# Kernel optimization log

Hardware: AMD Instinct MI355X
Metric: run time of the kernel (lower is better)

The kernel has to match this reference:

```python
import jax, jax.numpy as jnp
import numpy as np

B, OPI, RPI = 8, 64, 1024        # images, objects/image, rels/image
N, R = B * OPI, B * RPI           # 512 objects, 8192 relations
OBJ_DIM, H, T = 4096, 512, 3
NOC, NRC = 151, 51
IOU_THR = 0.3


def setup_inputs() -> dict:
    key = jax.random.key(0)
    ks = jax.random.split(key, 30)
    im_inds = jnp.repeat(jnp.arange(B, dtype=jnp.int64), OPI)
    rel_im = jnp.repeat(jnp.arange(B, dtype=jnp.int64), RPI)
    sub = rel_im * OPI + jax.random.randint(ks[0], (R,), 0, OPI)
    obj = rel_im * OPI + jax.random.randint(ks[1], (R,), 0, OPI)
    rel_inds = jnp.stack([rel_im, sub, obj], axis=1)
    obj_fmaps = jax.random.normal(ks[2], (N, OBJ_DIM), jnp.float32)
    obj_logits = jax.random.normal(ks[3], (N, NOC), jnp.float32)
    vr = jax.random.normal(ks[4], (R, OBJ_DIM), jnp.float32)
    xy = jax.random.uniform(ks[5], (N, NOC, 2), jnp.float32) * 500.0
    wh = jax.random.uniform(ks[6], (N, NOC, 2), jnp.float32) * 100.0 + 1.0
    boxes_per_cls = jnp.concatenate([xy, xy + wh], axis=-1)  # valid x1y1x2y2

    def lin(k, i, o):
        return jax.random.normal(k, (i, o), jnp.float32) / np.sqrt(i).astype(np.float32)

    params = dict(
        W_obj_proj=lin(ks[7], OBJ_DIM, H), b_obj_proj=jnp.zeros((H,), jnp.float32),
        W_rel_proj=lin(ks[8], OBJ_DIM, H), b_rel_proj=jnp.zeros((H,), jnp.float32),
        W_emb=lin(ks[9], NOC, H),
        W_msg_rel=lin(ks[10], H, H), W_msg_obj=lin(ks[11], H, H),
        W_gru_obj=lin(ks[12], H, 3 * H), U_gru_obj=lin(ks[13], H, 3 * H), b_gru_obj=jnp.zeros((3 * H,), jnp.float32),
        W_gru_rel=lin(ks[14], H, 3 * H), U_gru_rel=lin(ks[15], H, 3 * H), b_gru_rel=jnp.zeros((3 * H,), jnp.float32),
        W_cls_rel=lin(ks[16], H, NRC), b_cls_rel=jnp.zeros((NRC,), jnp.float32),
        W_cls_obj=lin(ks[17], H, NOC), b_cls_obj=jnp.zeros((NOC,), jnp.float32),
    )
    return dict(im_inds=im_inds, obj_fmaps=obj_fmaps, obj_logits=obj_logits,
                rel_inds=rel_inds, vr=vr, boxes_per_cls=boxes_per_cls, **params)


def _gru(h, x, W, U, b):
    g = jax.nn.sigmoid(x @ W[:, :2 * H] + h @ U[:, :2 * H] + b[:2 * H])
    z, r = jnp.split(g, 2, axis=-1)
    n = jnp.tanh(x @ W[:, 2 * H:] + (r * h) @ U[:, 2 * H:] + b[2 * H:])
    return (1.0 - z) * h + z * n


def _ggnn_image(rel_pair, obj_probs, obj_f, vr_im, W_emb, W_msg_rel, W_msg_obj,
                W_gru_obj, U_gru_obj, b_gru_obj, W_gru_rel, U_gru_rel, b_gru_rel,
                W_cls_rel, b_cls_rel, W_cls_obj, b_cls_obj):
    # object node init: projected features + class-prob embedding; rel nodes from vr
    h_obj = obj_f + obj_probs @ W_emb           # [OPI, H]
    h_rel = vr_im                                # [RPI, H]
    s, o = rel_pair[:, 0], rel_pair[:, 1]
    for _ in range(T):
        m_rel = (h_obj[s] + h_obj[o]) @ W_msg_rel
        hm = h_rel @ W_msg_obj
        m_obj = jnp.zeros_like(h_obj).at[s].add(hm).at[o].add(hm)
        h_rel = _gru(h_rel, m_rel, W_gru_rel, U_gru_rel, b_gru_rel)
        h_obj = _gru(h_obj, m_obj, W_gru_obj, U_gru_obj, b_gru_obj)
    return h_rel @ W_cls_rel + b_cls_rel, h_obj @ W_cls_obj + b_cls_obj


def _nms_keep(boxes, scores):
    # greedy NMS, iou_threshold=0.3; returns bool keep mask [N]
    order = jnp.argsort(-scores)
    b = boxes[order]
    area = (b[:, 2] - b[:, 0]) * (b[:, 3] - b[:, 1])
    lt = jnp.maximum(b[:, None, :2], b[None, :, :2])
    rb = jnp.minimum(b[:, None, 2:], b[None, :, 2:])
    wh = jnp.clip(rb - lt, 0.0)
    inter = wh[..., 0] * wh[..., 1]
    iou = inter / (area[:, None] + area[None, :] - inter + 1e-9)
    idx = jnp.arange(N)

    def body(i, keep):
        sup = keep[i] & (iou[i] > IOU_THR) & (idx > i)
        return keep & ~sup

    keep_sorted = jax.lax.fori_loop(0, N, body, jnp.ones((N,), bool))
    return jnp.zeros((N,), bool).at[order].set(keep_sorted)


def reference(im_inds, obj_fmaps, obj_logits, rel_inds, vr, boxes_per_cls,
              W_obj_proj, b_obj_proj, W_rel_proj, b_rel_proj, W_emb,
              W_msg_rel, W_msg_obj, W_gru_obj, U_gru_obj, b_gru_obj,
              W_gru_rel, U_gru_rel, b_gru_rel, W_cls_rel, b_cls_rel,
              W_cls_obj, b_cls_obj):
    obj_probs = jax.nn.softmax(obj_logits, axis=-1)
    fo = obj_fmaps @ W_obj_proj + b_obj_proj      # [N, H]
    vrp = vr @ W_rel_proj + b_rel_proj            # [R, H]
    # local object indices per image (rel_inds[:,1:] - obj_s), ragged -> uniform reshape
    rel_local = (rel_inds[:, 1:] - rel_inds[:, 0:1] * OPI).reshape(B, RPI, 2)
    ggnn = jax.vmap(_ggnn_image, in_axes=(0, 0, 0, 0) + (None,) * 13)
    rel_logits, obj_ref = ggnn(rel_local, obj_probs.reshape(B, OPI, NOC),
                               fo.reshape(B, OPI, H), vrp.reshape(B, RPI, H),
                               W_emb, W_msg_rel, W_msg_obj,
                               W_gru_obj, U_gru_obj, b_gru_obj,
                               W_gru_rel, U_gru_rel, b_gru_rel,
                               W_cls_rel, b_cls_rel, W_cls_obj, b_cls_obj)
    rel_logits = rel_logits.reshape(R, NRC)
    obj_logits_out = obj_ref.reshape(N, NOC)      # refine_obj_cls=True path
    obj_probs2 = jax.nn.softmax(obj_logits_out, axis=-1)
    # sgdet eval: per-class NMS (classes 1..NOC-1), vectorized over classes
    sp = jax.lax.stop_gradient(obj_probs2)        # .data in torch
    keep = jax.vmap(_nms_keep, in_axes=(1, 1))(boxes_per_cls[:, 1:], sp[:, 1:])  # [NOC-1, N]
    nms_mask = jnp.zeros((N, NOC), jnp.float32).at[:, 1:].set(keep.T.astype(jnp.float32))
    obj_preds = jnp.argmax((nms_mask * sp)[:, 1:], axis=1) + 1
    return obj_logits_out, obj_preds, rel_logits
```

## Files before the change

### kernel.cpp

```cpp
#include <hip/hip_runtime.h>
#include <math.h>

#define OPI 64
#define RPI 1024
#define N_OBJ 512
#define R_REL 8192
#define OBJ_DIM 4096
#define H 512
#define NOC 151
#define NRC 51
#define T_ITERS 3
#define IOU_THRESH 0.3f

typedef unsigned short u16;
typedef unsigned int u32;
typedef __attribute__((ext_vector_type(4))) float f32x4;
typedef __attribute__((ext_vector_type(8))) short bf16x8;
typedef __attribute__((ext_vector_type(2))) unsigned int u32x2;
typedef __attribute__((ext_vector_type(8))) short s16x8;

enum { EPI_STORE = 0, EPI_BIAS = 1, EPI_GATE = 3, EPI_NEWH = 4 };

__device__ inline u16 f2bf(float x) {
  u32 u = __float_as_uint(x);
  u32 r = (u + 0x7fffu + ((u >> 16) & 1u)) >> 16;
  return (u16)r;
}
__device__ inline float bf2f(u16 h) { return __uint_as_float(((u32)h) << 16); }
__device__ inline u32 cvtpk(float a, float b) {
  u32 r;
  asm("v_cvt_pk_bf16_f32 %0, %1, %2" : "=v"(r) : "v"(a), "v"(b));
  return r;
}

__global__ __launch_bounds__(256) void prep_bt(
    const float* __restrict__ W1, int ld1, int K1,
    const float* __restrict__ W2, int ld2, int K2,
    int coloff, int ncols, int N, int Kpad,
    u16* __restrict__ outh, u16* __restrict__ outl)
{
  __shared__ float tile[64][65];
  const int k0 = blockIdx.x * 64;
  const int n0 = blockIdx.y * 64;
  const int t = threadIdx.x;
  const int lane = t & 63;
  const int w = t >> 6;
#pragma unroll
  for (int p = 0; p < 16; ++p) {
    int kl = w * 16 + p;
    int k = k0 + kl;
    int n = n0 + lane;
    float v = 0.f;
    if (n < ncols) {
      if (k < K1) v = W1[(size_t)k * ld1 + coloff + n];
      else if (k - K1 < K2) v = W2[(size_t)(k - K1) * ld2 + coloff + n];
    }
    tile[kl][lane] = v;
  }
  __syncthreads();
#pragma unroll
  for (int p = 0; p < 16; ++p) {
    int nl = w * 16 + p;
    int n = n0 + nl;
    int k = k0 + lane;
    if (n < N && k < Kpad) {
      float v = tile[lane][nl];
      u16 h = f2bf(v);
      outh[(size_t)n * Kpad + k] = h;
      outl[(size_t)n * Kpad + k] = f2bf(v - bf2f(h));
    }
  }
}

template<int EPI, bool DUAL, bool GATHER, bool PAIR, bool SPLIT>
__global__ __launch_bounds__(256, 2) void mgemm_k(
    int M, int N, int K1, int K2, int nkt,
    const float* __restrict__ A1, int lda1,
    const float* __restrict__ A2, int lda2,
    const u16* __restrict__ Bth, const u16* __restrict__ Btl,
    const u16* __restrict__ Bth2, const u16* __restrict__ Btl2,
    const float* __restrict__ bias,
    float* __restrict__ C, int ldc, float* __restrict__ C2,
    const int* __restrict__ ridx,
    const float* __restrict__ Hb, int ldh,
    const float* __restrict__ Zin,
    float* __restrict__ Zout, float* __restrict__ RHout,
    float* __restrict__ part, int ktchunk)
{
  __shared__ u16 lAh[2][128 * 32];
  __shared__ u16 lAl[2][128 * 32];
  __shared__ u16 lBh[2][128 * 32];
  __shared__ u16 lBl[2][128 * 32];
  const int t = threadIdx.x;
  const int lane = t & 63;
  const int wid = t >> 6;
  const int wm = wid >> 1;
  const int wn = wid & 1;

  const int nbx = gridDim.x, nby = gridDim.y;
  const int nwg = nbx * nby;
  int orig = blockIdx.y * nbx + blockIdx.x;
  int lid = (orig & 7) * (nwg >> 3) + (orig >> 3);
  const int bx = lid % nbx;
  const int by = lid / nbx;

  const int m0 = by * 128;
  const int n0 = bx * 128;
  const int Kpad = nkt * 32;

  const float* A1p = A1; int ldap = lda1;
  const u16* Bhp = Bth; const u16* Blp = Btl;
  float* Cp = C;
  bool gath = GATHER;
  if (PAIR && blockIdx.z == 1) {
    A1p = A2; ldap = lda2; Bhp = Bth2; Blp = Btl2; Cp = C2; gath = false;
  }

  f32x4 acc[4][4];
#pragma unroll
  for (int m = 0; m < 4; ++m)
#pragma unroll
    for (int n = 0; n < 4; ++n) acc[m][n] = f32x4{0.f, 0.f, 0.f, 0.f};

  const int a_row = t >> 3;
  const int a_kq  = t & 7;
  int g_si[4], g_oi[4];
  if (gath) {
#pragma unroll
    for (int i = 0; i < 4; ++i) {
      int gm = m0 + a_row + i * 32;
      g_si[i] = ridx[gm * 3 + 1];
      g_oi[i] = ridx[gm * 3 + 2];
    }
  }
  const int b_row  = t >> 2;
  const int b_slot = t & 3;

  int ktb = 0, kte = nkt;
  if (SPLIT) {
    ktb = blockIdx.z * ktchunk;
    kte = min(nkt, ktb + ktchunk);
  }

  float4 rA[4];
  s16x8 rBh[2], rBl[2];

  auto loadA = [&](int kt) {
    const int gk = kt * 32 + a_kq * 4;
#pragma unroll
    for (int i = 0; i < 4; ++i) {
      const int gm = m0 + a_row + i * 32;
      if (gath) {
        float4 va = *(const float4*)&A1p[(size_t)g_si[i] * ldap + gk];
        float4 vb = *(const float4*)&A1p[(size_t)g_oi[i] * ldap + gk];
        rA[i] = make_float4(va.x + vb.x, va.y + vb.y, va.z + vb.z, va.w + vb.w);
      } else if (!DUAL) {
        rA[i] = *(const float4*)&A1p[(size_t)gm * ldap + gk];
      } else {
        if (gk + 3 < K1) {
          rA[i] = *(const float4*)&A1p[(size_t)gm * lda1 + gk];
        } else if (gk >= K1 && gk + 3 < K1 + K2 && (lda2 & 3) == 0) {
          rA[i] = *(const float4*)&A2[(size_t)gm * lda2 + (gk - K1)];
        } else {
          float xs[4];
#pragma unroll
          for (int e = 0; e < 4; ++e) {
            int gke = gk + e;
            float xv = 0.f;
            if (gke < K1) xv = A1p[(size_t)gm * lda1 + gke];
            else if (gke < K1 + K2) xv = A2[(size_t)gm * lda2 + (gke - K1)];
            xs[e] = xv;
          }
          rA[i] = make_float4(xs[0], xs[1], xs[2], xs[3]);
        }
      }
    }
  };
  auto loadB = [&](int kt) {
#pragma unroll
    for (int i = 0; i < 2; ++i) {
      const size_t goff = (size_t)(n0 + b_row + i * 64) * Kpad + kt * 32 + b_slot * 8;
      rBh[i] = *(const s16x8*)&Bhp[goff];
      rBl[i] = *(const s16x8*)&Blp[goff];
    }
  };
  auto stage = [&](int buf) {
#pragma unroll
    for (int i = 0; i < 4; ++i) {
      const int row = a_row + i * 32;
      float x0 = rA[i].x, x1 = rA[i].y, x2 = rA[i].z, x3 = rA[i].w;
      u32 h01 = cvtpk(x0, x1);
      u32 h23 = cvtpk(x2, x3);
      float r0 = __uint_as_float(h01 << 16);
      float r1 = __uint_as_float(h01 & 0xffff0000u);
      float r2 = __uint_as_float(h23 << 16);
      float r3 = __uint_as_float(h23 & 0xffff0000u);
      u32 l01 = cvtpk(x0 - r0, x1 - r1);
      u32 l23 = cvtpk(x2 - r2, x3 - r3);
      const int base = row * 32 + (((a_kq >> 1) ^ ((row >> 1) & 3)) << 3) + (a_kq & 1) * 4;
      *reinterpret_cast<u32x2*>(&lAh[buf][base]) = u32x2{h01, h23};
      *reinterpret_cast<u32x2*>(&lAl[buf][base]) = u32x2{l01, l23};
    }
#pragma unroll
    for (int i = 0; i < 2; ++i) {
      const int row = b_row + i * 64;
      const int base = row * 32 + ((b_slot ^ ((row >> 1) & 3)) << 3);
      *reinterpret_cast<s16x8*>(&lBh[buf][base]) = rBh[i];
      *reinterpret_cast<s16x8*>(&lBl[buf][base]) = rBl[i];
    }
  };

  const int fr = lane & 15;
  const int kg = lane >> 4;

  if (ktb < kte) {
    loadA(ktb);
    loadB(ktb);
    stage(0);
    __syncthreads();
    const int nk = kte - ktb;
    for (int kk = 0; kk < nk; ++kk) {
      const int cur = kk & 1;
      const bool more = (kk + 1 < nk);
      if (more) { loadA(ktb + kk + 1); loadB(ktb + kk + 1); }
      bf16x8 ah[4], al[4], bh[4], bl[4];
#pragma unroll
      for (int m = 0; m < 4; ++m) {
        const int r = wm * 64 + m * 16 + fr;
        const int addr = r * 32 + ((kg ^ ((r >> 1) & 3)) << 3);
        ah[m] = *reinterpret_cast<const bf16x8*>(&lAh[cur][addr]);
        al[m] = *reinterpret_cast<const bf16x8*>(&lAl[cur][addr]);
      }
#pragma unroll
      for (int n = 0; n < 4; ++n) {
        const int r = wn * 64 + n * 16 + fr;
        const int addr = r * 32 + ((kg ^ ((r >> 1) & 3)) << 3);
        bh[n] = *reinterpret_cast<const bf16x8*>(&lBh[cur][addr]);
        bl[n] = *reinterpret_cast<const bf16x8*>(&lBl[cur][addr]);
      }
      __builtin_amdgcn_s_setprio(1);
#pragma unroll
      for (int m = 0; m < 4; ++m)
#pragma unroll
        for (int n = 0; n < 4; ++n) {
          acc[m][n] = __builtin_amdgcn_mfma_f32_16x16x32_bf16(ah[m], bh[n], acc[m][n], 0, 0, 0);
          acc[m][n] = __builtin_amdgcn_mfma_f32_16x16x32_bf16(ah[m], bl[n], acc[m][n], 0, 0, 0);
          acc[m][n] = __builtin_amdgcn_mfma_f32_16x16x32_bf16(al[m], bh[n], acc[m][n], 0, 0, 0);
        }
      __builtin_amdgcn_s_setprio(0);
      if (more) stage(cur ^ 1);
      __syncthreads();
    }
  }

  const int col = lane & 15;
  const int rb = (lane >> 4) * 4;
  if (SPLIT) {
    const int Npad = gridDim.x * 128;
    float* pp = part + (size_t)blockIdx.z * M * Npad;
#pragma unroll
    for (int m = 0; m < 4; ++m)
#pragma unroll
      for (int n = 0; n < 4; ++n) {
        const int gn = n0 + wn * 64 + n * 16 + col;
#pragma unroll
        for (int j = 0; j < 4; ++j) {
          const int gm = m0 + wm * 64 + m * 16 + rb + j;
          pp[(size_t)gm * Npad + gn] = acc[m][n][j];
        }
      }
    return;
  }
#pragma unroll
  for (int m = 0; m < 4; ++m) {
#pragma unroll
    for (int n = 0; n < 4; ++n) {
      const int gn = n0 + wn * 64 + n * 16 + col;
      if (gn >= N) continue;
#pragma unroll
      for (int j = 0; j < 4; ++j) {
        const int gm = m0 + wm * 64 + m * 16 + rb + j;
        float v = acc[m][n][j];
        if (EPI == EPI_STORE) {
          Cp[(size_t)gm * ldc + gn] = v;
        } else if (EPI == EPI_BIAS) {
          Cp[(size_t)gm * ldc + gn] = v + bias[gn];
        } else if (EPI == EPI_GATE) {
          float g = 1.f / (1.f + expf(-(v + bias[gn])));
          int half = N >> 1;
          if (gn < half) Zout[(size_t)gm * half + gn] = g;
          else RHout[(size_t)gm * half + (gn - half)] = g * Hb[(size_t)gm * ldh + (gn - half)];
        } else if (EPI == EPI_NEWH) {
          float nv = tanhf(v + bias[gn]);
          float z = Zin[(size_t)gm * N + gn];
          float h = Hb[(size_t)gm * ldh + gn];
          Cp[(size_t)gm * ldc + gn] = (1.f - z) * h + z * nv;
        }
      }
    }
  }
}

template<int EPI>
__global__ __launch_bounds__(256) void epi_reduce(
    int S, int M, int N, int Npad,
    const float* __restrict__ part, const float* __restrict__ bias,
    float* __restrict__ C, int ldc,
    const float* __restrict__ Hb, int ldh,
    const float* __restrict__ Zin,
    float* __restrict__ Zout, float* __restrict__ RHout)
{
  int idx = blockIdx.x * 256 + threadIdx.x;
  if (idx >= M * Npad) return;
  int m = idx / Npad;
  int n = idx - m * Npad;
  if (n >= N) return;
  size_t stride = (size_t)M * Npad;
  float v = 0.f;
  for (int s = 0; s < S; ++s) v += part[s * stride + idx];
  if (EPI == EPI_BIAS) {
    C[(size_t)m * ldc + n] = v + bias[n];
  } else if (EPI == EPI_GATE) {
    float g = 1.f / (1.f + expf(-(v + bias[n])));
    int half = N >> 1;
    if (n < half) Zout[(size_t)m * half + n] = g;
    else RHout[(size_t)m * half + (n - half)] = g * Hb[(size_t)m * ldh + (n - half)];
  } else if (EPI == EPI_NEWH) {
    float nv = tanhf(v + bias[n]);
    float z = Zin[(size_t)m * N + n];
    float h = Hb[(size_t)m * ldh + n];
    C[(size_t)m * ldc + n] = (1.f - z) * h + z * nv;
  }
}

__global__ __launch_bounds__(256) void softmax_k(const float* __restrict__ X,
                                                 float* __restrict__ P)
{
  int row = blockIdx.x;
  int t = threadIdx.x;
  __shared__ float red[4];
  float x = (t < NOC) ? X[row * NOC + t] : -3.4e38f;
  float m = x;
#pragma unroll
  for (int o = 32; o > 0; o >>= 1) m = fmaxf(m, __shfl_xor(m, o, 64));
  if ((t & 63) == 0) red[t >> 6] = m;
  __syncthreads();
  float mm = fmaxf(fmaxf(red[0], red[1]), fmaxf(red[2], red[3]));
  float e = (t < NOC) ? expf(x - mm) : 0.f;
  float s = e;
#pragma unroll
  for (int o = 32; o > 0; o >>= 1) s += __shfl_xor(s, o, 64);
  __syncthreads();
  if ((t & 63) == 0) red[t >> 6] = s;
  __syncthreads();
  float ss = red[0] + red[1] + red[2] + red[3];
  if (t < NOC) P[row * NOC + t] = e / ss;
}

__global__ __launch_bounds__(256) void m_obj_gather_k(const float* __restrict__ hm,
                                                      const int* __restrict__ ridx,
                                                      float* __restrict__ m_obj)
{
  int n = blockIdx.x;
  int im = n >> 6;
  int col = threadIdx.x;
  float acc0 = 0.f, acc1 = 0.f;
  int r0 = im * RPI, r1 = r0 + RPI;
  for (int r = r0; r < r1; ++r) {
    int s = ridx[r * 3 + 1];
    int o = ridx[r * 3 + 2];
    int cnt = (s == n) + (o == n);
    if (cnt) {
      float f = (float)cnt;
      acc0 = fmaf(f, hm[r * H + col], acc0);
      acc1 = fmaf(f, hm[r * H + col + 256], acc1);
    }
  }
  m_obj[n * H + col] = acc0;
  m_obj[n * H + col + 256] = acc1;
}

__global__ __launch_bounds__(512) void nms_k(const float* __restrict__ probs2,
                                             const float* __restrict__ boxes,
                                             float* __restrict__ keepmask)
{
  int c = blockIdx.x + 1;
  int t = threadIdx.x;
  __shared__ float sc[512];
  __shared__ int   si[512];
  __shared__ float bx0[512], by0[512], bx1[512], by1[512], sar[512];
  __shared__ int   skeep[512];

  sc[t] = probs2[t * NOC + c];
  si[t] = t;
  __syncthreads();

  for (int k = 2; k <= 512; k <<= 1) {
    for (int j = k >> 1; j > 0; j >>= 1) {
      int p = t ^ j;
      if (p > t) {
        float s1 = sc[t], s2 = sc[p];
        int   i1 = si[t], i2 = si[p];
        bool tBefore = (s1 > s2) || (s1 == s2 && i1 < i2);
        bool up = ((t & k) == 0);
        if (up != tBefore) { sc[t] = s2; sc[p] = s1; si[t] = i2; si[p] = i1; }
      }
      __syncthreads();
    }
  }

  {
    const float* b = &boxes[(si[t] * NOC + c) * 4];
    float x0 = b[0], y0 = b[1], x1 = b[2], y1 = b[3];
    bx0[t] = x0; by0[t] = y0; bx1[t] = x1; by1[t] = y1;
    sar[t] = (x1 - x0) * (y1 - y0);
    skeep[t] = 1;
  }
  __syncthreads();

  for (int i = 0; i < 511; ++i) {
    if (skeep[i] && t > i && skeep[t]) {
      float lx = fmaxf(bx0[i], bx0[t]);
      float ly = fmaxf(by0[i], by0[t]);
      float rx = fminf(bx1[i], bx1[t]);
      float ry = fminf(by1[i], by1[t]);
      float w = fmaxf(rx - lx, 0.f);
      float h = fmaxf(ry - ly, 0.f);
      float inter = w * h;
      float iou = inter / (sar[i] + sar[t] - inter + 1e-9f);
      if (iou > IOU_THRESH) skeep[t] = 0;
    }
    __syncthreads();
  }

  keepmask[(c - 1) * N_OBJ + si[t]] = skeep[t] ? 1.f : 0.f;
}

__global__ void pred_k(const float* __restrict__ probs2,
                       const float* __restrict__ keepmask,
                       float* __restrict__ out)
{
  int i = threadIdx.x + blockIdx.x * 256;
  if (i >= N_OBJ) return;
  float best = -1.f;
  int bc = 0;
  for (int c = 0; c < NOC - 1; ++c) {
    float v = keepmask[c * N_OBJ + i] * probs2[i * NOC + c + 1];
    if (v > best) { best = v; bc = c; }
  }
  out[i] = (float)(bc + 1);
}

extern "C" void kernel_launch(void* const* d_in, const int* in_sizes, int n_in,
                              void* d_out, int out_size, void* d_ws, size_t ws_size,
                              hipStream_t stream) {
  const float* obj_fmaps  = (const float*)d_in[1];
  const float* obj_logits = (const float*)d_in[2];
  const int*   rel_inds   = (const int*)d_in[3];
  const float* vr         = (const float*)d_in[4];
  const float* boxes      = (const float*)d_in[5];
  const float* W_obj_proj = (const float*)d_in[6];
  const float* b_obj_proj = (const float*)d_in[7];
  const float* W_rel_proj = (const float*)d_in[8];
  const float* b_rel_proj = (const float*)d_in[9];
  const float* W_emb      = (const float*)d_in[10];
  const float* W_msg_rel  = (const float*)d_in[11];
  const float* W_msg_obj  = (const float*)d_in[12];
  const float* W_gru_obj  = (const float*)d_in[13];
  const float* U_gru_obj  = (const float*)d_in[14];
  const float* b_gru_obj  = (const float*)d_in[15];
  const float* W_gru_rel  = (const float*)d_in[16];
  const float* U_gru_rel  = (const float*)d_in[17];
  const float* b_gru_rel  = (const float*)d_in[18];
  const float* W_cls_rel  = (const float*)d_in[19];
  const float* b_cls_rel  = (const float*)d_in[20];
  const float* W_cls_obj  = (const float*)d_in[21];
  const float* b_cls_obj  = (const float*)d_in[22];

  float* ws = (float*)d_ws;
  const size_t RH = (size_t)R_REL * H;
  const size_t NH = (size_t)N_OBJ * H;
  float* h_rel  = ws;
  float* m_rel  = h_rel  + RH;
  float* z_rel  = m_rel  + RH;
  float* rh_rel = z_rel  + RH;
  float* h_obj  = rh_rel + RH;
  float* m_obj  = h_obj  + NH;
  float* z_obj  = m_obj  + NH;
  float* rh_obj = z_obj  + NH;
  float* obj_probs  = rh_obj + NH;
  float* obj_probs2 = obj_probs  + (size_t)N_OBJ * NOC;
  float* keepmask   = obj_probs2 + (size_t)N_OBJ * NOC;
  float* hm   = z_rel;
  float* part = m_rel;
  float* fend = keepmask + (size_t)(NOC - 1) * N_OBJ;

  u16* bt = (u16*)fend;
  const int KP_HOBJ = 4256;
  const int KP_HREL = 4096;
  const int KP_MSG  = 512;
  const int KP_GRU  = 1024;
  const int KP_CLS  = 512;
  u16* p = bt;
  u16* bt_hobj_h = p; p += (size_t)H * KP_HOBJ;      u16* bt_hobj_l = p; p += (size_t)H * KP_HOBJ;
  u16* bt_hrel_h = p; p += (size_t)H * KP_HREL;      u16* bt_hrel_l = p; p += (size_t)H * KP_HREL;
  u16* bt_mrel_h = p; p += (size_t)H * KP_MSG;       u16* bt_mrel_l = p; p += (size_t)H * KP_MSG;
  u16* bt_hm_h   = p; p += (size_t)H * KP_MSG;       u16* bt_hm_l   = p; p += (size_t)H * KP_MSG;
  u16* bt_gr_h   = p; p += (size_t)2 * H * KP_GRU;   u16* bt_gr_l   = p; p += (size_t)2 * H * KP_GRU;
  u16* bt_nr_h   = p; p += (size_t)H * KP_GRU;       u16* bt_nr_l   = p; p += (size_t)H * KP_GRU;
  u16* bt_go_h   = p; p += (size_t)2 * H * KP_GRU;   u16* bt_go_l   = p; p += (size_t)2 * H * KP_GRU;
  u16* bt_no_h   = p; p += (size_t)H * KP_GRU;       u16* bt_no_l   = p; p += (size_t)H * KP_GRU;
  u16* bt_cr_h   = p; p += (size_t)128 * KP_CLS;     u16* bt_cr_l   = p; p += (size_t)128 * KP_CLS;
  u16* bt_co_h   = p; p += (size_t)256 * KP_CLS;     u16* bt_co_l   = p; p += (size_t)256 * KP_CLS;

  size_t used_b = (size_t)((char*)p - (char*)d_ws);
  used_b = (used_b + 15) & ~(size_t)15;
  float* part2 = (float*)((char*)d_ws + used_b);
  bool have2 = (used_b + 2 * RH * sizeof(float)) <= ws_size;

  float* out_logits = (float*)d_out;
  float* out_preds  = out_logits + (size_t)N_OBJ * NOC;
  float* out_rel    = out_preds + N_OBJ;

  dim3 blk(256);
#define PREP(W1, ld1, K1, W2, ld2, K2, coff, NC, NN, KP, oh, ol) \
  prep_bt<<<dim3(((KP) + 63) / 64, ((NN) + 63) / 64), 256, 0, stream>>>( \
      W1, ld1, K1, W2, ld2, K2, coff, NC, NN, KP, oh, ol)

  PREP(W_obj_proj, H, OBJ_DIM, W_emb, H, NOC, 0, H, H, KP_HOBJ, bt_hobj_h, bt_hobj_l);
  PREP(W_rel_proj, H, OBJ_DIM, (const float*)nullptr, 0, 0, 0, H, H, KP_HREL, bt_hrel_h, bt_hrel_l);
  PREP(W_msg_rel, H, H, (const float*)nullptr, 0, 0, 0, H, H, KP_MSG, bt_mrel_h, bt_mrel_l);
  PREP(W_msg_obj, H, H, (const float*)nullptr, 0, 0, 0, H, H, KP_MSG, bt_hm_h, bt_hm_l);
  PREP(W_gru_rel, 3 * H, H, U_gru_rel, 3 * H, H, 0, 2 * H, 2 * H, KP_GRU, bt_gr_h, bt_gr_l);
  PREP(W_gru_rel, 3 * H, H, U_gru_rel, 3 * H, H, 2 * H, H, H, KP_GRU, bt_nr_h, bt_nr_l);
  PREP(W_gru_obj, 3 * H, H, U_gru_obj, 3 * H, H, 0, 2 * H, 2 * H, KP_GRU, bt_go_h, bt_go_l);
  PREP(W_gru_obj, 3 * H, H, U_gru_obj, 3 * H, H, 2 * H, H, H, KP_GRU, bt_no_h, bt_no_l);
  PREP(W_cls_rel, NRC, H, (const float*)nullptr, 0, 0, 0, NRC, 128, KP_CLS, bt_cr_h, bt_cr_l);
  PREP(W_cls_obj, NOC, H, (const float*)nullptr, 0, 0, 0, NOC, 256, KP_CLS, bt_co_h, bt_co_l);

  softmax_k<<<N_OBJ, 256, 0, stream>>>(obj_logits, obj_probs);

#define MG(EPI, DUAL, GATH, PAIR, SPLIT, grid, M, N, K1, K2, nkt, A1, lda1, A2, lda2, \
           Bh, Bl, Bh2, Bl2, bias, C, ldc, C2, ridx, Hb, ldh, Zin, Zo, RHo, part, ktc) \
  mgemm_k<EPI, DUAL, GATH, PAIR, SPLIT><<<grid, blk, 0, stream>>>( \
      M, N, K1, K2, nkt, A1, lda1, A2, lda2, Bh, Bl, Bh2, Bl2, bias, C, ldc, C2, \
      ridx, Hb, ldh, Zin, Zo, RHo, part, ktc)

  MG(EPI_STORE, true, false, false, true, dim3(4, 4, 8), N_OBJ, H, OBJ_DIM, NOC, KP_HOBJ / 32,
     obj_fmaps, OBJ_DIM, obj_probs, NOC, bt_hobj_h, bt_hobj_l, nullptr, nullptr,
     nullptr, nullptr, 0, nullptr, nullptr, nullptr, 0, nullptr, nullptr, nullptr, part, 17);
  epi_reduce<EPI_BIAS><<<(N_OBJ * H + 255) / 256, blk, 0, stream>>>(
      8, N_OBJ, H, H, part, b_obj_proj, h_obj, H, nullptr, 0, nullptr, nullptr, nullptr);

  MG(EPI_STORE, false, false, false, true, dim3(4, 64, 2), R_REL, H, OBJ_DIM, 0, KP_HREL / 32,
     vr, OBJ_DIM, nullptr, 0, bt_hrel_h, bt_hrel_l, nullptr, nullptr,
     nullptr, nullptr, 0, nullptr, nullptr, nullptr, 0, nullptr, nullptr, nullptr, part, 64);
  epi_reduce<EPI_BIAS><<<((int)(RH) + 255) / 256, blk, 0, stream>>>(
      2, R_REL, H, H, part, b_rel_proj, h_rel, H, nullptr, 0, nullptr, nullptr, nullptr);

  for (int it = 0; it < T_ITERS; ++it) {
    MG(EPI_STORE, false, true, true, false, dim3(4, 64, 2), R_REL, H, H, 0, KP_MSG / 32,
       h_obj, H, h_rel, H, bt_mrel_h, bt_mrel_l, bt_hm_h, bt_hm_l,
       nullptr, m_rel, H, hm, rel_inds, nullptr, 0, nullptr, nullptr, nullptr, nullptr, 0);
    m_obj_gather_k<<<N_OBJ, 256, 0, stream>>>(hm, rel_inds, m_obj);

    MG(EPI_GATE, true, false, false, false, dim3(8, 64), R_REL, 2 * H, H, H, KP_GRU / 32,
       m_rel, H, h_rel, H, bt_gr_h, bt_gr_l, nullptr, nullptr,
       b_gru_rel, nullptr, 0, nullptr, nullptr, h_rel, H, nullptr, z_rel, rh_rel, nullptr, 0);
    if (have2) {
      MG(EPI_STORE, true, false, false, true, dim3(4, 64, 2), R_REL, H, H, H, KP_GRU / 32,
         m_rel, H, rh_rel, H, bt_nr_h, bt_nr_l, nullptr, nullptr,
         nullptr, nullptr, 0, nullptr, nullptr, nullptr, 0, nullptr, nullptr, nullptr, part2, 16);
      epi_reduce<EPI_NEWH><<<((int)(RH) + 255) / 256, blk, 0, stream>>>(
          2, R_REL, H, H, part2, b_gru_rel + 2 * H, h_rel, H, h_rel, H, z_rel, nullptr, nullptr);
    } else {
      MG(EPI_NEWH, true, false, false, false, dim3(4, 64), R_REL, H, H, H, KP_GRU / 32,
         m_rel, H, rh_rel, H, bt_nr_h, bt_nr_l, nullptr, nullptr,
         b_gru_rel + 2 * H, h_rel, H, nullptr, nullptr, h_rel, H, z_rel, nullptr, nullptr, nullptr, 0);
    }

    MG(EPI_STORE, true, false, false, true, dim3(8, 4, 8), N_OBJ, 2 * H, H, H, KP_GRU / 32,
       m_obj, H, h_obj, H, bt_go_h, bt_go_l, nullptr, nullptr,
       nullptr, nullptr, 0, nullptr, nullptr, nullptr, 0, nullptr, nullptr, nullptr, part, 4);
    epi_reduce<EPI_GATE><<<(N_OBJ * 2 * H + 255) / 256, blk, 0, stream>>>(
        8, N_OBJ, 2 * H, 2 * H, part, b_gru_obj, nullptr, 0, h_obj, H, nullptr, z_obj, rh_obj);
    MG(EPI_STORE, true, false, false, true, dim3(4, 4, 8), N_OBJ, H, H, H, KP_GRU / 32,
       m_obj, H, rh_obj, H, bt_no_h, bt_no_l, nullptr, nullptr,
       nullptr, nullptr, 0, nullptr, nullptr, nullptr, 0, nullptr, nullptr, nullptr, part, 4);
    epi_reduce<EPI_NEWH><<<(N_OBJ * H + 255) / 256, blk, 0, stream>>>(
        8, N_OBJ, H, H, part, b_gru_obj + 2 * H, h_obj, H, h_obj, H, z_obj, nullptr, nullptr);
  }

  MG(EPI_STORE, false, false, false, true, dim3(1, 64, 4), R_REL, NRC, H, 0, KP_CLS / 32,
     h_rel, H, nullptr, 0, bt_cr_h, bt_cr_l, nullptr, nullptr,
     nullptr, nullptr, 0, nullptr, nullptr, nullptr, 0, nullptr, nullptr, nullptr, part, 4);
  epi_reduce<EPI_BIAS><<<(R_REL * 128 + 255) / 256, blk, 0, stream>>>(
      4, R_REL, NRC, 128, part, b_cls_rel, out_rel, NRC, nullptr, 0, nullptr, nullptr, nullptr);
  MG(EPI_STORE, false, false, false, true, dim3(2, 4, 8), N_OBJ, NOC, H, 0, KP_CLS / 32,
     h_obj, H, nullptr, 0, bt_co_h, bt_co_l, nullptr, nullptr,
     nullptr, nullptr, 0, nullptr, nullptr, nullptr, 0, nullptr, nullptr, nullptr, part, 2);
  epi_reduce<EPI_BIAS><<<(N_OBJ * 256 + 255) / 256, blk, 0, stream>>>(
      8, N_OBJ, NOC, 256, part, b_cls_obj, out_logits, NOC, nullptr, 0, nullptr, nullptr, nullptr);

  softmax_k<<<N_OBJ, 256, 0, stream>>>(out_logits, obj_probs2);
  nms_k<<<NOC - 1, 512, 0, stream>>>(obj_probs2, boxes, keepmask);
  pred_k<<<2, 256, 0, stream>>>(obj_probs2, keepmask, out_preds);
}
```

Before: 1.522 ms.

## Replace barrier-per-box NMS loop with bitmask IoU matrix and single-wave resolve

The old NMS ran 511 serial steps, each ending in a block-wide barrier. Now every thread first computes its row of the pairwise IoU matrix against all other boxes and packs the suppression results into 64-bit words in shared memory. A single wavefront then resolves the keep bits by walking the boxes in order, using lane shuffles and no block barriers. This removes most of the synchronisation, but it computes the full 512x512 IoU matrix (more divides) and uses more shared memory, and the resolve step is still a 512-step serial chain.

```diff
diff --git a/kernel.cpp b/kernel.cpp
--- a/kernel.cpp
+++ b/kernel.cpp
@@ -14,6 +14,7 @@
 
 typedef unsigned short u16;
 typedef unsigned int u32;
+typedef unsigned long long u64;
 typedef __attribute__((ext_vector_type(4))) float f32x4;
 typedef __attribute__((ext_vector_type(8))) short bf16x8;
 typedef __attribute__((ext_vector_type(2))) unsigned int u32x2;
@@ -389,7 +390,8 @@
   __shared__ float sc[512];
   __shared__ int   si[512];
   __shared__ float bx0[512], by0[512], bx1[512], by1[512], sar[512];
-  __shared__ int   skeep[512];
+  __shared__ u64   msk[512][8];
+  __shared__ u64   keepw_s[8];
 
   sc[t] = probs2[t * NOC + c];
   si[t] = t;
@@ -414,26 +416,48 @@
     float x0 = b[0], y0 = b[1], x1 = b[2], y1 = b[3];
     bx0[t] = x0; by0[t] = y0; bx1[t] = x1; by1[t] = y1;
     sar[t] = (x1 - x0) * (y1 - y0);
-    skeep[t] = 1;
-  }
-  __syncthreads();
-
-  for (int i = 0; i < 511; ++i) {
-    if (skeep[i] && t > i && skeep[t]) {
-      float lx = fmaxf(bx0[i], bx0[t]);
-      float ly = fmaxf(by0[i], by0[t]);
-      float rx = fminf(bx1[i], bx1[t]);
-      float ry = fminf(by1[i], by1[t]);
-      float w = fmaxf(rx - lx, 0.f);
-      float h = fmaxf(ry - ly, 0.f);
-      float inter = w * h;
-      float iou = inter / (sar[i] + sar[t] - inter + 1e-9f);
-      if (iou > IOU_THRESH) skeep[t] = 0;
-    }
-    __syncthreads();
-  }
-
-  keepmask[(c - 1) * N_OBJ + si[t]] = skeep[t] ? 1.f : 0.f;
+  }
+  __syncthreads();
+
+  {
+    const float x0 = bx0[t], y0 = by0[t], x1 = bx1[t], y1 = by1[t], ar = sar[t];
+#pragma unroll
+    for (int w = 0; w < 8; ++w) {
+      u64 bits = 0ull;
+#pragma unroll 4
+      for (int b = 0; b < 64; ++b) {
+        const int j = w * 64 + b;
+        float lx = fmaxf(x0, bx0[j]);
+        float ly = fmaxf(y0, by0[j]);
+        float rx = fminf(x1, bx1[j]);
+        float ry = fminf(y1, by1[j]);
+        float ww = fmaxf(rx - lx, 0.f);
+        float hh = fmaxf(ry - ly, 0.f);
+        float inter = ww * hh;
+        float iou = inter / (ar + sar[j] - inter + 1e-9f);
+        bits |= ((u64)((j > t) && (iou > IOU_THRESH))) << b;
+      }
+      msk[t][w] = bits;
+    }
+  }
+  __syncthreads();
+
+  if (t < 64) {
+    const int w = t & 7;
+    u64 keepw = ~0ull;
+    u64 m = msk[0][w];
+    for (int i = 0; i < 512; ++i) {
+      u64 mn = (i + 1 < 512) ? msk[i + 1][w] : 0ull;
+      u64 kw = __shfl(keepw, i >> 6, 64);
+      if ((kw >> (i & 63)) & 1ull) keepw &= ~m;
+      m = mn;
+    }
+    if (t < 8) keepw_s[t] = keepw;
+  }
+  __syncthreads();
+
+  const u64 kw = keepw_s[t >> 6];
+  keepmask[(c - 1) * N_OBJ + si[t]] = ((kw >> (t & 63)) & 1ull) ? 1.f : 0.f;
 }
 
 __global__ void pred_k(const float* __restrict__ probs2,
```

Result: no change. 1.498 ms (-1.6%).
